# Kernel tuning notes

Measured on AMD Instinct MI355X. Metric: run time of the kernel, lower is better.

The kernel has to match this reference:

```python
import jax, jax.numpy as jnp
import numpy as np

C_IN = 256
C_RED = max(4, C_IN // 4)  # 64


def setup_inputs() -> dict:
    key = jax.random.key(0)
    k1, k2, k3, k4, k5 = jax.random.split(key, 5)
    B, C, H, W = 4, C_IN, 64, 64
    x = jax.random.normal(k1, (B, C, H, W), dtype=jnp.float32)
    # 1x1 convs (no bias) are just channel matmuls: weight shape (out_ch, in_ch)
    s_in = 1.0 / np.sqrt(C)
    s_red = 1.0 / np.sqrt(C_RED)
    Wq = jax.random.normal(k2, (C_RED, C), dtype=jnp.float32) * s_in
    Wk = jax.random.normal(k3, (C_RED, C), dtype=jnp.float32) * s_in
    Wv = jax.random.normal(k4, (C_RED, C), dtype=jnp.float32) * s_in
    Wp = jax.random.normal(k5, (C, C_RED), dtype=jnp.float32) * s_red
    return {"x": x, "Wq": Wq, "Wk": Wk, "Wv": Wv, "Wp": Wp}


def reference(x, Wq, Wk, Wv, Wp):
    B, C, H, W = x.shape
    N = H * W
    xf = x.reshape(B, C, N)                       # (B, C, N)
    q = jnp.einsum('rc,bcn->bnr', Wq, xf)         # (B, N, c_red)
    k = jnp.einsum('rc,bcn->brn', Wk, xf)         # (B, c_red, N)
    v = jnp.einsum('rc,bcn->bnr', Wv, xf)         # (B, N, c_red)
    scale = 1.0 / jnp.sqrt(jnp.float32(k.shape[1]))
    attn = jnp.einsum('bnr,brm->bnm', q, k) * scale   # (B, N, N)
    attn = jax.nn.softmax(attn, axis=-1)
    out = jnp.einsum('bnm,bmr->brn', attn, v)     # (B, c_red, N)
    out = jnp.einsum('cr,brn->bcn', Wp, out)      # (B, C, N)
    return out.reshape(B, C, H, W) + x
```

## Files before the change

kernel.cpp:

```cpp
#include <hip/hip_runtime.h>
#include <hip/hip_bf16.h>

#define CIN 256
#define CRED 64
#define NB 4
#define NN 4096

typedef float v4f __attribute__((ext_vector_type(4)));
typedef short v8s __attribute__((ext_vector_type(8)));
typedef unsigned short u16;
typedef u16 u16x4 __attribute__((ext_vector_type(4)));
typedef u16 u16x8 __attribute__((ext_vector_type(8)));
typedef unsigned int u32;

#define LOG2E 1.4426950408889634f

__device__ __forceinline__ u16 f2bf(float f) {
    union { float f; u32 u; } v; v.f = f;
    u32 r = (v.u + 0x7FFFu + ((v.u >> 16) & 1u)) >> 16;
    return (u16)r;
}
__device__ __forceinline__ float bf2f(u16 s) {
    union { u32 u; float f; } v; v.u = ((u32)s) << 16;
    return v.f;
}
__device__ __forceinline__ u32 pkbf(float a, float b) {
    float2 f; f.x = a; f.y = b;
    __hip_bfloat162 h = __float22bfloat162_rn(f);
    union { __hip_bfloat162 h; u32 u; } c; c.h = h;
    return c.u;
}
__device__ __forceinline__ v4f mfma16(v8s a, v8s b, v4f c) {
    return __builtin_amdgcn_mfma_f32_16x16x32_bf16(a, b, c, 0, 0, 0);
}
__device__ __forceinline__ float fexp2(float x) {
#if __has_builtin(__builtin_amdgcn_exp2f)
    return __builtin_amdgcn_exp2f(x);
#else
    return exp2f(x);
#endif
}

__global__ __launch_bounds__(256) void k_qkvm(const float* __restrict__ x,
                                              const float* __restrict__ Wq,
                                              const float* __restrict__ Wk,
                                              const float* __restrict__ Wv,
                                              u16* __restrict__ Q, u16* __restrict__ K,
                                              u16* __restrict__ V) {
    int t = threadIdx.x;
    int wv = t >> 6, lane = t & 63, c15 = lane & 15, quad = lane >> 4;
    int mat = blockIdx.x >> 9;
    int sub = blockIdx.x & 511;
    int b = sub >> 7;
    int nb = (sub & 127) * 32;
    const float* xb = x + ((size_t)b << 20);
    const float* W = (mat == 0) ? Wq : (mat == 1) ? Wk : Wv;
    float s = (mat == 0) ? (0.125f * LOG2E) : 1.0f;

    v8s Af[2][8];
#pragma unroll
    for (int nt = 0; nt < 2; ++nt) {
        const float* px = xb + nb + nt * 16 + c15 + (size_t)quad * 8 * 4096;
#pragma unroll
        for (int kc = 0; kc < 8; ++kc) {
            float f[8];
#pragma unroll
            for (int j = 0; j < 8; ++j)
                f[j] = px[((size_t)kc * 32 + j) * 4096];
            union { v8s s; u32 w[4]; } pk;
            pk.w[0] = pkbf(f[0], f[1]); pk.w[1] = pkbf(f[2], f[3]);
            pk.w[2] = pkbf(f[4], f[5]); pk.w[3] = pkbf(f[6], f[7]);
            Af[nt][kc] = pk.s;
        }
    }

    v8s Bf[8];
    {
        const float* wr = W + (size_t)(wv * 16 + c15) * 256 + quad * 8;
#pragma unroll
        for (int kc = 0; kc < 8; ++kc) {
            float4 a = *(const float4*)&wr[kc * 32];
            float4 c = *(const float4*)&wr[kc * 32 + 4];
            union { v8s s; u32 w[4]; } pk;
            pk.w[0] = pkbf(a.x * s, a.y * s); pk.w[1] = pkbf(a.z * s, a.w * s);
            pk.w[2] = pkbf(c.x * s, c.y * s); pk.w[3] = pkbf(c.z * s, c.w * s);
            Bf[kc] = pk.s;
        }
    }

#pragma unroll
    for (int nt = 0; nt < 2; ++nt) {
        v4f acc = {0.f, 0.f, 0.f, 0.f};
#pragma unroll
        for (int kc = 0; kc < 8; ++kc)
            acc = mfma16(Af[nt][kc], Bf[kc], acc);
        if (mat < 2) {
            u16* base = (mat == 0) ? Q : K;
            u16* dst = base + ((size_t)b << 18)
                     + (size_t)(nb + nt * 16 + quad * 4) * 64
                     + wv * 16 + c15;
#pragma unroll
            for (int g = 0; g < 4; ++g) dst[g * 64] = f2bf(acc[g]);
        } else {
            int hi2 = ((nb + nt * 16) >> 4) & 3;
            size_t base = ((size_t)b * 64 + wv * 16 + c15) * 4096
                        + (size_t)((nb + nt * 16) & ~63) + hi2;
#pragma unroll
            for (int g = 0; g < 4; ++g)
                V[base + (quad * 4 + g) * 4] = f2bf(acc[g]);
        }
    }
}

__global__ __launch_bounds__(256, 2) void k_flash(const u16* __restrict__ Q,
                                                  const u16* __restrict__ K,
                                                  const u16* __restrict__ V,
                                                  u16* __restrict__ OP,
                                                  float* __restrict__ Lb,
                                                  int sh) {
    __shared__ u16 Kl[2][64][72];
    __shared__ u16 Vl[2][64][72];
    __shared__ u16 Pl[4][32][72];
    int t = threadIdx.x;
    int p = blockIdx.x & ((1u << sh) - 1);
    int tile = blockIdx.x >> sh;
    int b = tile >> 5;
    int n0 = (tile & 31) * 128;
    int wv = t >> 6;
    int lane = t & 63;
    int c15 = lane & 15;
    int quad = lane >> 4;
    int nw = n0 + wv * 32;
    const u16* Qb = Q + (size_t)b * NN * 64;
    const u16* Kb = K + (size_t)b * NN * 64;
    const u16* Vb = V + (size_t)b * 64 * NN;

    v8s Qa[2][2];
#pragma unroll
    for (int rg = 0; rg < 2; ++rg)
#pragma unroll
        for (int c2 = 0; c2 < 2; ++c2)
            Qa[rg][c2] = *(const v8s*)&Qb[(size_t)(nw + rg * 16 + c15) * 64 + c2 * 32 + quad * 8];

    v4f O[2][4];
    float ls[2][4];
#pragma unroll
    for (int rg = 0; rg < 2; ++rg)
#pragma unroll
        for (int g = 0; g < 4; ++g) {
            ls[rg][g] = 0.f;
#pragma unroll
            for (int cg = 0; cg < 4; ++cg) O[rg][cg][g] = 0.f;
        }

    int mlen = NN >> sh;
    int m0 = p * mlen;
    int iters = mlen >> 6;
    int srow = t >> 3, scol = (t & 7) * 8;

#pragma unroll
    for (int pass = 0; pass < 2; ++pass) {
        int rr = srow + pass * 32;
        *(v8s*)&Kl[0][rr][scol] = *(const v8s*)&Kb[(size_t)(m0 + rr) * 64 + scol];
        *(v8s*)&Vl[0][rr][scol] = *(const v8s*)&Vb[(size_t)rr * NN + m0 + scol];
    }
    __syncthreads();

    for (int it = 0; it < iters; ++it) {
        int cur = it & 1, nxt = cur ^ 1;

        v8s kn[2], vn[2];
        if (it + 1 < iters) {
            int mt = m0 + (it + 1) * 64;
#pragma unroll
            for (int pass = 0; pass < 2; ++pass) {
                int rr = srow + pass * 32;
                kn[pass] = *(const v8s*)&Kb[(size_t)(mt + rr) * 64 + scol];
                vn[pass] = *(const v8s*)&Vb[(size_t)rr * NN + mt + scol];
            }
        }

        v4f S[2][4];
#pragma unroll
        for (int rg = 0; rg < 2; ++rg)
#pragma unroll
            for (int s = 0; s < 4; ++s)
#pragma unroll
                for (int g = 0; g < 4; ++g) S[rg][s][g] = 0.f;
#pragma unroll
        for (int s = 0; s < 4; ++s)
#pragma unroll
            for (int c2 = 0; c2 < 2; ++c2) {
                v8s kb = *(const v8s*)&Kl[cur][s * 16 + c15][c2 * 32 + quad * 8];
                S[0][s] = mfma16(Qa[0][c2], kb, S[0][s]);
                S[1][s] = mfma16(Qa[1][c2], kb, S[1][s]);
            }

#pragma unroll
        for (int rg = 0; rg < 2; ++rg) {
            float E[4][4];
#pragma unroll
            for (int s = 0; s < 4; ++s)
#pragma unroll
                for (int g = 0; g < 4; ++g) {
                    float e = fexp2(S[rg][s][g]);
                    E[s][g] = e;
                    ls[rg][g] += e;
                }
#pragma unroll
            for (int g = 0; g < 4; ++g) {
                union { u16x4 v; u32 w[2]; } p2;
                p2.w[0] = pkbf(E[0][g], E[1][g]);
                p2.w[1] = pkbf(E[2][g], E[3][g]);
                *(u16x4*)&Pl[wv][rg * 16 + quad * 4 + g][c15 * 4] = p2.v;
            }
        }

        v8s Pa[2][2];
#pragma unroll
        for (int rg = 0; rg < 2; ++rg)
#pragma unroll
            for (int c2 = 0; c2 < 2; ++c2)
                Pa[rg][c2] = *(const v8s*)&Pl[wv][rg * 16 + c15][c2 * 32 + quad * 8];
#pragma unroll
        for (int cg = 0; cg < 4; ++cg)
#pragma unroll
            for (int c2 = 0; c2 < 2; ++c2) {
                v8s vb = *(const v8s*)&Vl[cur][cg * 16 + c15][c2 * 32 + quad * 8];
                O[0][cg] = mfma16(Pa[0][c2], vb, O[0][cg]);
                O[1][cg] = mfma16(Pa[1][c2], vb, O[1][cg]);
            }

        if (it + 1 < iters) {
#pragma unroll
            for (int pass = 0; pass < 2; ++pass) {
                int rr = srow + pass * 32;
                *(v8s*)&Kl[nxt][rr][scol] = kn[pass];
                *(v8s*)&Vl[nxt][rr][scol] = vn[pass];
            }
        }
        __syncthreads();
    }

    u16* OPp = OP + (size_t)p * (NB * NN * 64) + (size_t)b * NN * 64;
#pragma unroll
    for (int rg = 0; rg < 2; ++rg)
#pragma unroll
        for (int cg = 0; cg < 4; ++cg)
#pragma unroll
            for (int g = 0; g < 4; ++g) {
                int n = nw + rg * 16 + quad * 4 + g;
                OPp[(size_t)n * 64 + cg * 16 + c15] = f2bf(O[rg][cg][g]);
            }
#pragma unroll
    for (int rg = 0; rg < 2; ++rg)
#pragma unroll
        for (int g = 0; g < 4; ++g) {
            float v = ls[rg][g];
#pragma unroll
            for (int off = 1; off <= 8; off <<= 1) v += __shfl_xor(v, off);
            ls[rg][g] = v;
        }
    if (c15 == 0) {
        float* Lp = Lb + (size_t)p * (NB * NN) + (size_t)b * NN;
#pragma unroll
        for (int rg = 0; rg < 2; ++rg)
#pragma unroll
            for (int g = 0; g < 4; ++g) {
                int n = nw + rg * 16 + quad * 4 + g;
                Lp[n] = ls[rg][g];
            }
    }
}

#define OMP 72
__global__ __launch_bounds__(256) void k_proj(const u16* __restrict__ OP,
                                              const float* __restrict__ Lb,
                                              const float* __restrict__ Wp,
                                              const float* __restrict__ x,
                                              float* __restrict__ out,
                                              int nsp) {
    __shared__ u16 Om[16 * OMP];
    int t = threadIdx.x;
    int b = blockIdx.x >> 8;
    int n0 = (blockIdx.x & 255) * 16;

    {
        int n_l = t >> 4, r0 = (t & 15) * 4;
        size_t nidx = (size_t)b * NN + n0 + n_l;
        float o[4] = {0.f, 0.f, 0.f, 0.f};
        float l = 0.f;
        for (int p = 0; p < nsp; ++p) {
            u16x4 u = *(const u16x4*)&OP[((size_t)p * (NB * NN) + nidx) * 64 + r0];
#pragma unroll
            for (int j = 0; j < 4; ++j) o[j] += bf2f(u[j]);
            l += Lb[(size_t)p * (NB * NN) + nidx];
        }
        float inv = 1.0f / l;
        union { u16x4 v; u32 w[2]; } p2;
        p2.w[0] = pkbf(o[0] * inv, o[1] * inv);
        p2.w[1] = pkbf(o[2] * inv, o[3] * inv);
        *(u16x4*)&Om[n_l * OMP + r0] = p2.v;
    }
    __syncthreads();

    int lane = t & 63, wvv = t >> 6, c15 = lane & 15, quad = lane >> 4;
    v8s B0 = *(const v8s*)&Om[c15 * OMP + quad * 8];
    v8s B1 = *(const v8s*)&Om[c15 * OMP + 32 + quad * 8];
#pragma unroll
    for (int ct0 = 0; ct0 < 4; ++ct0) {
        int ct = wvv * 4 + ct0;
        const float* wr = Wp + (size_t)(ct * 16 + c15) * 64 + quad * 8;
        float4 wa = *(const float4*)&wr[0];
        float4 wb = *(const float4*)&wr[4];
        float4 wc = *(const float4*)&wr[32];
        float4 wd = *(const float4*)&wr[36];
        union { v8s s; u32 w[4]; } pa, pb;
        pa.w[0] = pkbf(wa.x, wa.y); pa.w[1] = pkbf(wa.z, wa.w);
        pa.w[2] = pkbf(wb.x, wb.y); pa.w[3] = pkbf(wb.z, wb.w);
        pb.w[0] = pkbf(wc.x, wc.y); pb.w[1] = pkbf(wc.z, wc.w);
        pb.w[2] = pkbf(wd.x, wd.y); pb.w[3] = pkbf(wd.z, wd.w);
        v4f acc = {0.f, 0.f, 0.f, 0.f};
        acc = mfma16(pa.s, B0, acc);
        acc = mfma16(pb.s, B1, acc);
        size_t base = ((size_t)(b * 256 + ct * 16 + quad * 4)) * 4096 + n0 + c15;
#pragma unroll
        for (int g = 0; g < 4; ++g)
            out[base + (size_t)g * 4096] = acc[g] + x[base + (size_t)g * 4096];
    }
}

extern "C" void kernel_launch(void* const* d_in, const int* in_sizes, int n_in,
                              void* d_out, int out_size, void* d_ws, size_t ws_size,
                              hipStream_t stream) {
    const float* x  = (const float*)d_in[0];
    const float* Wq = (const float*)d_in[1];
    const float* Wk = (const float*)d_in[2];
    const float* Wv = (const float*)d_in[3];
    const float* Wp = (const float*)d_in[4];
    float* out = (float*)d_out;
    char* ws = (char*)d_ws;

    int nsp = (ws_size >= (size_t)24 * 1024 * 1024) ? 8 : 4;
    int sh = (nsp == 8) ? 3 : 2;

    u16* Q   = (u16*)(ws);
    u16* K   = (u16*)(ws + 2097152);
    u16* V   = (u16*)(ws + 2 * 2097152);
    u16* OP  = (u16*)(ws + 3 * 2097152);
    float* Lbuf = (float*)(ws + (size_t)(3 + nsp) * 2097152);

    k_qkvm<<<1536, 256, 0, stream>>>(x, Wq, Wk, Wv, Q, K, V);
    k_flash<<<NB * 32 * nsp, 256, 0, stream>>>(Q, K, V, OP, Lbuf, sh);
    k_proj<<<NB * 256, 256, 0, stream>>>(OP, Lbuf, Wp, x, out, nsp);
}
```

Baseline: 136.1 us.

## Compute Q/K/V in one block per column tile and stream V directly from global

The projection kernel now has each block load its x tile once and produce all three of Q, K and V, with each wave handling three 16-row output tiles. This cuts the launch to a third of the blocks and stops x being re-read for each matrix. The flash kernel drops the V shared-memory buffer and loads V fragments straight from global memory into registers, split into two halves that are issued before the QK and softmax phases so the loads overlap compute. Freeing that shared memory allows launch bounds of 4 blocks per CU. The trade-off is more VGPR pressure and possibly uncoalesced, latency-exposed global V reads on every iteration.

```diff
diff --git a/kernel.cpp b/kernel.cpp
--- a/kernel.cpp
+++ b/kernel.cpp
@@ -49,13 +49,9 @@
                                               u16* __restrict__ V) {
     int t = threadIdx.x;
     int wv = t >> 6, lane = t & 63, c15 = lane & 15, quad = lane >> 4;
-    int mat = blockIdx.x >> 9;
-    int sub = blockIdx.x & 511;
-    int b = sub >> 7;
-    int nb = (sub & 127) * 32;
+    int n0g = blockIdx.x * 32;
+    int b = n0g >> 12, nb = n0g & 4095;
     const float* xb = x + ((size_t)b << 20);
-    const float* W = (mat == 0) ? Wq : (mat == 1) ? Wk : Wv;
-    float s = (mat == 0) ? (0.125f * LOG2E) : 1.0f;
 
     v8s Af[2][8];
 #pragma unroll
@@ -74,9 +70,13 @@
         }
     }
 
-    v8s Bf[8];
-    {
-        const float* wr = W + (size_t)(wv * 16 + c15) * 256 + quad * 8;
+#pragma unroll
+    for (int rti = 0; rti < 3; ++rti) {
+        int rt = wv * 3 + rti;
+        const float* W = (rt < 4) ? Wq : (rt < 8) ? Wk : Wv;
+        float s = (rt < 4) ? (0.125f * LOG2E) : 1.0f;
+        const float* wr = W + (size_t)((rt & 3) * 16 + c15) * 256 + quad * 8;
+        v8s Bf[8];
 #pragma unroll
         for (int kc = 0; kc < 8; ++kc) {
             float4 a = *(const float4*)&wr[kc * 32];
@@ -86,40 +86,38 @@
             pk.w[2] = pkbf(c.x * s, c.y * s); pk.w[3] = pkbf(c.z * s, c.w * s);
             Bf[kc] = pk.s;
         }
-    }
-
-#pragma unroll
-    for (int nt = 0; nt < 2; ++nt) {
-        v4f acc = {0.f, 0.f, 0.f, 0.f};
-#pragma unroll
-        for (int kc = 0; kc < 8; ++kc)
-            acc = mfma16(Af[nt][kc], Bf[kc], acc);
-        if (mat < 2) {
-            u16* base = (mat == 0) ? Q : K;
-            u16* dst = base + ((size_t)b << 18)
-                     + (size_t)(nb + nt * 16 + quad * 4) * 64
-                     + wv * 16 + c15;
-#pragma unroll
-            for (int g = 0; g < 4; ++g) dst[g * 64] = f2bf(acc[g]);
-        } else {
-            int hi2 = ((nb + nt * 16) >> 4) & 3;
-            size_t base = ((size_t)b * 64 + wv * 16 + c15) * 4096
-                        + (size_t)((nb + nt * 16) & ~63) + hi2;
-#pragma unroll
-            for (int g = 0; g < 4; ++g)
-                V[base + (quad * 4 + g) * 4] = f2bf(acc[g]);
-        }
-    }
-}
-
-__global__ __launch_bounds__(256, 2) void k_flash(const u16* __restrict__ Q,
+#pragma unroll
+        for (int nt = 0; nt < 2; ++nt) {
+            v4f acc = {0.f, 0.f, 0.f, 0.f};
+#pragma unroll
+            for (int kc = 0; kc < 8; ++kc)
+                acc = mfma16(Af[nt][kc], Bf[kc], acc);
+            if (rt < 8) {
+                u16* base = (rt < 4) ? Q : K;
+                u16* dst = base + ((size_t)b << 18)
+                         + (size_t)(nb + nt * 16 + quad * 4) * 64
+                         + (rt & 3) * 16 + c15;
+#pragma unroll
+                for (int g = 0; g < 4; ++g) dst[g * 64] = f2bf(acc[g]);
+            } else {
+                int hi2 = ((nb + nt * 16) >> 4) & 3;
+                size_t base = ((size_t)b * 64 + (rt - 8) * 16 + c15) * 4096
+                            + (size_t)((nb + nt * 16) & ~63) + hi2;
+#pragma unroll
+                for (int g = 0; g < 4; ++g)
+                    V[base + (quad * 4 + g) * 4] = f2bf(acc[g]);
+            }
+        }
+    }
+}
+
+__global__ __launch_bounds__(256, 4) void k_flash(const u16* __restrict__ Q,
                                                   const u16* __restrict__ K,
                                                   const u16* __restrict__ V,
                                                   u16* __restrict__ OP,
                                                   float* __restrict__ Lb,
                                                   int sh) {
     __shared__ u16 Kl[2][64][72];
-    __shared__ u16 Vl[2][64][72];
     __shared__ u16 Pl[4][32][72];
     int t = threadIdx.x;
     int p = blockIdx.x & ((1u << sh) - 1);
@@ -162,23 +160,28 @@
     for (int pass = 0; pass < 2; ++pass) {
         int rr = srow + pass * 32;
         *(v8s*)&Kl[0][rr][scol] = *(const v8s*)&Kb[(size_t)(m0 + rr) * 64 + scol];
-        *(v8s*)&Vl[0][rr][scol] = *(const v8s*)&Vb[(size_t)rr * NN + m0 + scol];
     }
     __syncthreads();
 
     for (int it = 0; it < iters; ++it) {
         int cur = it & 1, nxt = cur ^ 1;
-
-        v8s kn[2], vn[2];
+        int mt = m0 + it * 64;
+
+        v8s kn[2];
         if (it + 1 < iters) {
-            int mt = m0 + (it + 1) * 64;
+            int mt1 = mt + 64;
 #pragma unroll
             for (int pass = 0; pass < 2; ++pass) {
                 int rr = srow + pass * 32;
-                kn[pass] = *(const v8s*)&Kb[(size_t)(mt + rr) * 64 + scol];
-                vn[pass] = *(const v8s*)&Vb[(size_t)rr * NN + mt + scol];
-            }
-        }
+                kn[pass] = *(const v8s*)&Kb[(size_t)(mt1 + rr) * 64 + scol];
+            }
+        }
+        v8s vd0[2][2];
+#pragma unroll
+        for (int cg = 0; cg < 2; ++cg)
+#pragma unroll
+            for (int c2 = 0; c2 < 2; ++c2)
+                vd0[cg][c2] = *(const v8s*)&Vb[(size_t)(cg * 16 + c15) * NN + mt + c2 * 32 + quad * 8];
 
         v4f S[2][4];
 #pragma unroll
@@ -195,6 +198,13 @@
                 S[0][s] = mfma16(Qa[0][c2], kb, S[0][s]);
                 S[1][s] = mfma16(Qa[1][c2], kb, S[1][s]);
             }
+
+        v8s vd1[2][2];
+#pragma unroll
+        for (int cg = 0; cg < 2; ++cg)
+#pragma unroll
+            for (int c2 = 0; c2 < 2; ++c2)
+                vd1[cg][c2] = *(const v8s*)&Vb[(size_t)((cg + 2) * 16 + c15) * NN + mt + c2 * 32 + quad * 8];
 
 #pragma unroll
         for (int rg = 0; rg < 2; ++rg) {
@@ -223,12 +233,13 @@
             for (int c2 = 0; c2 < 2; ++c2)
                 Pa[rg][c2] = *(const v8s*)&Pl[wv][rg * 16 + c15][c2 * 32 + quad * 8];
 #pragma unroll
-        for (int cg = 0; cg < 4; ++cg)
+        for (int cg = 0; cg < 2; ++cg)
 #pragma unroll
             for (int c2 = 0; c2 < 2; ++c2) {
-                v8s vb = *(const v8s*)&Vl[cur][cg * 16 + c15][c2 * 32 + quad * 8];
-                O[0][cg] = mfma16(Pa[0][c2], vb, O[0][cg]);
-                O[1][cg] = mfma16(Pa[1][c2], vb, O[1][cg]);
+                O[0][cg] = mfma16(Pa[0][c2], vd0[cg][c2], O[0][cg]);
+                O[1][cg] = mfma16(Pa[1][c2], vd0[cg][c2], O[1][cg]);
+                O[0][cg + 2] = mfma16(Pa[0][c2], vd1[cg][c2], O[0][cg + 2]);
+                O[1][cg + 2] = mfma16(Pa[1][c2], vd1[cg][c2], O[1][cg + 2]);
             }
 
         if (it + 1 < iters) {
@@ -236,7 +247,6 @@
             for (int pass = 0; pass < 2; ++pass) {
                 int rr = srow + pass * 32;
                 *(v8s*)&Kl[nxt][rr][scol] = kn[pass];
-                *(v8s*)&Vl[nxt][rr][scol] = vn[pass];
             }
         }
         __syncthreads();
@@ -350,7 +360,7 @@
     u16* OP  = (u16*)(ws + 3 * 2097152);
     float* Lbuf = (float*)(ws + (size_t)(3 + nsp) * 2097152);
 
-    k_qkvm<<<1536, 256, 0, stream>>>(x, Wq, Wk, Wv, Q, K, V);
+    k_qkvm<<<512, 256, 0, stream>>>(x, Wq, Wk, Wv, Q, K, V);
     k_flash<<<NB * 32 * nsp, 256, 0, stream>>>(Q, K, V, OP, Lbuf, sh);
     k_proj<<<NB * 256, 256, 0, stream>>>(OP, Lbuf, Wp, x, out, nsp);
 }
```

Measured after the change: 159.0 us. 16.9% more time.
